# Kernel tuning notes

Measured on AMD Instinct MI355X. Metric: run time of the kernel, lower is better.

## Reference

```python
import jax, jax.numpy as jnp
import numpy as np

N, E, F, H, C = 100000, 1600000, 32, 64, 10


def setup_inputs() -> dict:
    key = jax.random.key(0)
    ks = jax.random.split(key, 12)
    x = jax.random.normal(ks[0], (N, F), dtype=jnp.float32)
    edge_index = jax.random.randint(ks[1], (2, E), 0, N, dtype=jnp.int64)
    edge_attr = jax.random.uniform(ks[2], (E,), dtype=jnp.float32)
    s = lambda k, shp, fan: jax.random.normal(k, shp, dtype=jnp.float32) / np.sqrt(fan)
    return {
        "x": x,
        "edge_index": edge_index,
        "edge_attr": edge_attr,
        "W1_rel": s(ks[3], (H, F), F),
        "b1_rel": jnp.zeros((H,), jnp.float32),
        "W1_root": s(ks[4], (H, F), F),
        "W2_rel": s(ks[5], (H, H), H),
        "b2_rel": jnp.zeros((H,), jnp.float32),
        "W2_root": s(ks[6], (H, H), H),
        "fc_w": s(ks[7], (C, H), H),
        "fc_b": jnp.zeros((C,), jnp.float32),
    }


def graph_conv(x, src, dst, ew, W_rel, b_rel, W_root):
    # message: x_j * e_ji, scatter-add at destination nodes (PyG GraphConv, aggr='add')
    msg = x[src] * ew[:, None]            # [E, d] gather + scale
    agg = jax.ops.segment_sum(msg, dst, num_segments=N)  # [N, d]
    return agg @ W_rel.T + b_rel + x @ W_root.T


def reference(x, edge_index, edge_attr, W1_rel, b1_rel, W1_root, W2_rel, b2_rel, W2_root, fc_w, fc_b):
    src, dst = edge_index[0], edge_index[1]
    h = jax.nn.relu(graph_conv(x, src, dst, edge_attr, W1_rel, b1_rel, W1_root))
    h = jax.nn.relu(graph_conv(h, src, dst, edge_attr, W2_rel, b2_rel, W2_root))
    return h @ fc_w.T + fc_b
```

## Files before the change

kernel.cpp:

```cpp
#include <hip/hip_runtime.h>

#define N_NODES 100000
#define EDGES   1600000
#define F_IN    32
#define H_DIM   64
#define C_OUT   10
#define SCAN_NB ((N_NODES + 511) / 512)

__global__ __launch_bounds__(256) void hist_kernel(
    const int* __restrict__ ei, int* __restrict__ cnt)
{
    int e = blockIdx.x * 256 + threadIdx.x;
    if (e >= EDGES) return;
    atomicAdd(&cnt[ei[EDGES + e]], 1);
}

__global__ __launch_bounds__(512) void scan1_kernel(
    const int* __restrict__ cnt, int* __restrict__ part, int* __restrict__ bsum)
{
    __shared__ int s[512];
    int tid = threadIdx.x;
    int gid = blockIdx.x * 512 + tid;
    int v = (gid < N_NODES) ? cnt[gid] : 0;
    s[tid] = v;
    __syncthreads();
    for (int off = 1; off < 512; off <<= 1) {
        int t = (tid >= off) ? s[tid - off] : 0;
        __syncthreads();
        s[tid] += t;
        __syncthreads();
    }
    if (gid < N_NODES) part[gid] = s[tid] - v;
    if (tid == 511) bsum[blockIdx.x] = s[511];
}

__global__ __launch_bounds__(256) void scan2_kernel(
    const int* __restrict__ bsum, int* __restrict__ bsumx)
{
    __shared__ int s[256];
    int tid = threadIdx.x;
    int v = (tid < SCAN_NB) ? bsum[tid] : 0;
    s[tid] = v;
    __syncthreads();
    for (int off = 1; off < 256; off <<= 1) {
        int t = (tid >= off) ? s[tid - off] : 0;
        __syncthreads();
        s[tid] += t;
        __syncthreads();
    }
    bsumx[tid] = s[tid] - v;
}

__global__ __launch_bounds__(512) void scan3_kernel(
    const int* __restrict__ part, const int* __restrict__ bsumx,
    int* __restrict__ offs, int* __restrict__ cursor)
{
    int gid = blockIdx.x * 512 + threadIdx.x;
    if (gid < N_NODES) {
        int o = part[gid] + bsumx[blockIdx.x];
        offs[gid] = o;
        cursor[gid] = o;
    }
    if (gid == 0) offs[N_NODES] = EDGES;
}

__global__ __launch_bounds__(256) void fill_kernel(
    const int* __restrict__ ei, const float* __restrict__ ew,
    int* __restrict__ cursor, uint2* __restrict__ bucket)
{
    int e = blockIdx.x * 256 + threadIdx.x;
    if (e >= EDGES) return;
    int d = ei[EDGES + e];
    int pos = atomicAdd(&cursor[d], 1);
    uint2 slot;
    slot.x = (unsigned)ei[e];
    slot.y = __float_as_uint(ew[e]);
    bucket[pos] = slot;
}

#define K1_NPB 8
__global__ __launch_bounds__(256) void agg_dense1_kernel(
    const float* __restrict__ x, const uint2* __restrict__ bucket,
    const int* __restrict__ offs,
    const float* __restrict__ W_rel, const float* __restrict__ b_rel,
    const float* __restrict__ W_root, float* __restrict__ h1)
{
    __shared__ float sWrel[64][33];
    __shared__ float sWroot[64][33];
    __shared__ float sb[64];
    __shared__ float sagg[K1_NPB][33];
    __shared__ float sx[K1_NPB][33];
    int tid = threadIdx.x;
    for (int i = tid; i < 64 * 32; i += 256) {
        sWrel[i >> 5][i & 31]  = W_rel[i];
        sWroot[i >> 5][i & 31] = W_root[i];
    }
    if (tid < 64) sb[tid] = b_rel[tid];
    int g = tid >> 5, f = tid & 31;
    int n4 = tid >> 6, h = tid & 63;

    for (int base = blockIdx.x * K1_NPB; base < N_NODES; base += gridDim.x * K1_NPB) {
        __syncthreads();
        {
            int node = base + g;
            float acc = 0.f, xv = 0.f;
            if (node < N_NODES) {
                xv = x[(size_t)node * 32 + f];
                int o0 = offs[node], o1 = offs[node + 1];
                int j = o0;
                for (; j + 4 <= o1; j += 4) {
                    uint2 s0 = bucket[j + 0];
                    uint2 s1 = bucket[j + 1];
                    uint2 s2 = bucket[j + 2];
                    uint2 s3 = bucket[j + 3];
                    float v0 = x[(size_t)s0.x * 32 + f];
                    float v1 = x[(size_t)s1.x * 32 + f];
                    float v2 = x[(size_t)s2.x * 32 + f];
                    float v3 = x[(size_t)s3.x * 32 + f];
                    acc += v0 * __uint_as_float(s0.y) + v1 * __uint_as_float(s1.y)
                         + v2 * __uint_as_float(s2.y) + v3 * __uint_as_float(s3.y);
                }
                for (; j < o1; ++j) {
                    uint2 s = bucket[j];
                    acc += x[(size_t)s.x * 32 + f] * __uint_as_float(s.y);
                }
            }
            sagg[g][f] = acc;
            sx[g][f] = xv;
        }
        __syncthreads();
        for (int ni = 0; ni < 2; ++ni) {
            int nn = ni * 4 + n4;
            int node = base + nn;
            if (node < N_NODES) {
                float sum = sb[h];
                #pragma unroll
                for (int ff = 0; ff < 32; ++ff)
                    sum += sagg[nn][ff] * sWrel[h][ff] + sx[nn][ff] * sWroot[h][ff];
                h1[(size_t)node * 64 + h] = fmaxf(sum, 0.f);
            }
        }
    }
}

#define K2_NPB 4
__global__ __launch_bounds__(256) void agg_dense2_kernel(
    const float* __restrict__ h1, const uint2* __restrict__ bucket,
    const int* __restrict__ offs,
    const float* __restrict__ W_rel, const float* __restrict__ b_rel,
    const float* __restrict__ W_root,
    const float* __restrict__ fc_w, const float* __restrict__ fc_b,
    float* __restrict__ out)
{
    __shared__ float sWrel[64][65];
    __shared__ float sWroot[64][65];
    __shared__ float sfc[10][65];
    __shared__ float sb[64], sfb[10];
    __shared__ float sagg[K2_NPB][65];
    __shared__ float sh[K2_NPB][65];
    __shared__ float sh2[K2_NPB][65];
    int tid = threadIdx.x;
    for (int i = tid; i < 64 * 64; i += 256) {
        sWrel[i >> 6][i & 63]  = W_rel[i];
        sWroot[i >> 6][i & 63] = W_root[i];
    }
    for (int i = tid; i < 10 * 64; i += 256) sfc[i >> 6][i & 63] = fc_w[i];
    if (tid < 64) sb[tid] = b_rel[tid];
    if (tid < 10) sfb[tid] = fc_b[tid];
    int g = tid >> 6, f = tid & 63;

    for (int base = blockIdx.x * K2_NPB; base < N_NODES; base += gridDim.x * K2_NPB) {
        __syncthreads();
        {
            int node = base + g;
            float acc = 0.f, hv = 0.f;
            if (node < N_NODES) {
                hv = h1[(size_t)node * 64 + f];
                int o0 = __builtin_amdgcn_readfirstlane(offs[node]);
                int o1 = __builtin_amdgcn_readfirstlane(offs[node + 1]);
                int j = o0;
                for (; j + 4 <= o1; j += 4) {
                    uint2 s0 = bucket[j + 0];
                    uint2 s1 = bucket[j + 1];
                    uint2 s2 = bucket[j + 2];
                    uint2 s3 = bucket[j + 3];
                    float v0 = h1[(size_t)s0.x * 64 + f];
                    float v1 = h1[(size_t)s1.x * 64 + f];
                    float v2 = h1[(size_t)s2.x * 64 + f];
                    float v3 = h1[(size_t)s3.x * 64 + f];
                    acc += v0 * __uint_as_float(s0.y) + v1 * __uint_as_float(s1.y)
                         + v2 * __uint_as_float(s2.y) + v3 * __uint_as_float(s3.y);
                }
                for (; j < o1; ++j) {
                    uint2 s = bucket[j];
                    acc += h1[(size_t)s.x * 64 + f] * __uint_as_float(s.y);
                }
            }
            sagg[g][f] = acc;
            sh[g][f] = hv;
        }
        __syncthreads();
        {
            float sum = sb[f];
            #pragma unroll
            for (int ff = 0; ff < 64; ++ff)
                sum += sagg[g][ff] * sWrel[f][ff] + sh[g][ff] * sWroot[f][ff];
            sh2[g][f] = fmaxf(sum, 0.f);
        }
        __syncthreads();
        if (tid < 4 * 10) {
            int n2 = tid / 10, c = tid % 10;
            int node = base + n2;
            if (node < N_NODES) {
                float o = sfb[c];
                #pragma unroll
                for (int ff = 0; ff < 64; ++ff)
                    o += sh2[n2][ff] * sfc[c][ff];
                out[(size_t)node * 10 + c] = o;
            }
        }
    }
}

extern "C" void kernel_launch(void* const* d_in, const int* in_sizes, int n_in,
                              void* d_out, int out_size, void* d_ws, size_t ws_size,
                              hipStream_t stream) {
    const float* x       = (const float*)d_in[0];
    const int*   ei      = (const int*)d_in[1];
    const float* ew      = (const float*)d_in[2];
    const float* W1_rel  = (const float*)d_in[3];
    const float* b1_rel  = (const float*)d_in[4];
    const float* W1_root = (const float*)d_in[5];
    const float* W2_rel  = (const float*)d_in[6];
    const float* b2_rel  = (const float*)d_in[7];
    const float* W2_root = (const float*)d_in[8];
    const float* fc_w    = (const float*)d_in[9];
    const float* fc_b    = (const float*)d_in[10];
    float* out = (float*)d_out;

    uint2* bucket = (uint2*)d_ws;
    float* h1     = (float*)(bucket + EDGES);
    int*   cnt    = (int*)(h1 + (size_t)N_NODES * 64);
    int*   part   = cnt + N_NODES;
    int*   offs   = part + N_NODES;
    int*   cursor = offs + N_NODES + 1;
    int*   bsum   = cursor + N_NODES;
    int*   bsumx  = bsum + 256;

    hipMemsetAsync(cnt, 0, (size_t)N_NODES * sizeof(int), stream);

    hist_kernel<<<(EDGES + 255) / 256, 256, 0, stream>>>(ei, cnt);
    scan1_kernel<<<SCAN_NB, 512, 0, stream>>>(cnt, part, bsum);
    scan2_kernel<<<1, 256, 0, stream>>>(bsum, bsumx);
    scan3_kernel<<<SCAN_NB, 512, 0, stream>>>(part, bsumx, offs, cursor);
    fill_kernel<<<(EDGES + 255) / 256, 256, 0, stream>>>(ei, ew, cursor, bucket);

    agg_dense1_kernel<<<2048, 256, 0, stream>>>(
        x, bucket, offs, W1_rel, b1_rel, W1_root, h1);
    agg_dense2_kernel<<<2048, 256, 0, stream>>>(
        h1, bucket, offs, W2_rel, b2_rel, W2_root, fc_w, fc_b, out);
}
```

Baseline: 502.6 us.

## Store hidden activations and weights in bf16, unroll gathers by eight

Stores the intermediate layer-1 output as bf16, halving the bytes gathered per edge in the second aggregation and the size of the h1 buffer. Weights are packed as bf16 pairs in shared memory, and both gather loops gain an 8-way unrolled path for more memory-level parallelism. Launch bounds now request higher occupancy. This gives up accuracy in the activations and weights, and each 2-byte gather per lane may coalesce less efficiently.

```diff
diff --git a/kernel.cpp b/kernel.cpp
--- a/kernel.cpp
+++ b/kernel.cpp
@@ -6,6 +6,16 @@
 #define H_DIM   64
 #define C_OUT   10
 #define SCAN_NB ((N_NODES + 511) / 512)
+
+__device__ __forceinline__ unsigned pack_bf16(float a, float b) {
+    unsigned ua = (__float_as_uint(a) + 0x8000u) >> 16;
+    unsigned ub = (__float_as_uint(b) + 0x8000u) & 0xffff0000u;
+    return ub | ua;
+}
+__device__ __forceinline__ float bflo(unsigned p) { return __uint_as_float(p << 16); }
+__device__ __forceinline__ float bfhi(unsigned p) { return __uint_as_float(p & 0xffff0000u); }
+__device__ __forceinline__ float bf2f(unsigned short u) { return __uint_as_float(((unsigned)u) << 16); }
+__device__ __forceinline__ unsigned short f2bf(float x) { return (unsigned short)((__float_as_uint(x) + 0x8000u) >> 16); }
 
 __global__ __launch_bounds__(256) void hist_kernel(
     const int* __restrict__ ei, int* __restrict__ cnt)
@@ -79,21 +89,22 @@
 }
 
 #define K1_NPB 8
-__global__ __launch_bounds__(256) void agg_dense1_kernel(
+__global__ __launch_bounds__(256, 6) void agg_dense1_kernel(
     const float* __restrict__ x, const uint2* __restrict__ bucket,
     const int* __restrict__ offs,
     const float* __restrict__ W_rel, const float* __restrict__ b_rel,
-    const float* __restrict__ W_root, float* __restrict__ h1)
-{
-    __shared__ float sWrel[64][33];
-    __shared__ float sWroot[64][33];
+    const float* __restrict__ W_root, unsigned short* __restrict__ h1b)
+{
+    __shared__ unsigned sWrel[64][17];
+    __shared__ unsigned sWroot[64][17];
     __shared__ float sb[64];
     __shared__ float sagg[K1_NPB][33];
     __shared__ float sx[K1_NPB][33];
     int tid = threadIdx.x;
-    for (int i = tid; i < 64 * 32; i += 256) {
-        sWrel[i >> 5][i & 31]  = W_rel[i];
-        sWroot[i >> 5][i & 31] = W_root[i];
+    for (int i = tid; i < 64 * 16; i += 256) {
+        int h = i >> 4, k = i & 15;
+        sWrel[h][k]  = pack_bf16(W_rel[h * 32 + 2 * k],  W_rel[h * 32 + 2 * k + 1]);
+        sWroot[h][k] = pack_bf16(W_root[h * 32 + 2 * k], W_root[h * 32 + 2 * k + 1]);
     }
     if (tid < 64) sb[tid] = b_rel[tid];
     int g = tid >> 5, f = tid & 31;
@@ -108,11 +119,27 @@
                 xv = x[(size_t)node * 32 + f];
                 int o0 = offs[node], o1 = offs[node + 1];
                 int j = o0;
+                for (; j + 8 <= o1; j += 8) {
+                    uint2 s0 = bucket[j + 0], s1 = bucket[j + 1];
+                    uint2 s2 = bucket[j + 2], s3 = bucket[j + 3];
+                    uint2 s4 = bucket[j + 4], s5 = bucket[j + 5];
+                    uint2 s6 = bucket[j + 6], s7 = bucket[j + 7];
+                    float v0 = x[(size_t)s0.x * 32 + f];
+                    float v1 = x[(size_t)s1.x * 32 + f];
+                    float v2 = x[(size_t)s2.x * 32 + f];
+                    float v3 = x[(size_t)s3.x * 32 + f];
+                    float v4 = x[(size_t)s4.x * 32 + f];
+                    float v5 = x[(size_t)s5.x * 32 + f];
+                    float v6 = x[(size_t)s6.x * 32 + f];
+                    float v7 = x[(size_t)s7.x * 32 + f];
+                    acc += v0 * __uint_as_float(s0.y) + v1 * __uint_as_float(s1.y)
+                         + v2 * __uint_as_float(s2.y) + v3 * __uint_as_float(s3.y)
+                         + v4 * __uint_as_float(s4.y) + v5 * __uint_as_float(s5.y)
+                         + v6 * __uint_as_float(s6.y) + v7 * __uint_as_float(s7.y);
+                }
                 for (; j + 4 <= o1; j += 4) {
-                    uint2 s0 = bucket[j + 0];
-                    uint2 s1 = bucket[j + 1];
-                    uint2 s2 = bucket[j + 2];
-                    uint2 s3 = bucket[j + 3];
+                    uint2 s0 = bucket[j + 0], s1 = bucket[j + 1];
+                    uint2 s2 = bucket[j + 2], s3 = bucket[j + 3];
                     float v0 = x[(size_t)s0.x * 32 + f];
                     float v1 = x[(size_t)s1.x * 32 + f];
                     float v2 = x[(size_t)s2.x * 32 + f];
@@ -135,36 +162,45 @@
             if (node < N_NODES) {
                 float sum = sb[h];
                 #pragma unroll
-                for (int ff = 0; ff < 32; ++ff)
-                    sum += sagg[nn][ff] * sWrel[h][ff] + sx[nn][ff] * sWroot[h][ff];
-                h1[(size_t)node * 64 + h] = fmaxf(sum, 0.f);
+                for (int k = 0; k < 16; ++k) {
+                    unsigned pr = sWrel[h][k], po = sWroot[h][k];
+                    sum += sagg[nn][2 * k]     * bflo(pr)
+                         + sagg[nn][2 * k + 1] * bfhi(pr)
+                         + sx[nn][2 * k]       * bflo(po)
+                         + sx[nn][2 * k + 1]   * bfhi(po);
+                }
+                h1b[(size_t)node * 64 + h] = f2bf(fmaxf(sum, 0.f));
             }
         }
     }
 }
 
 #define K2_NPB 4
-__global__ __launch_bounds__(256) void agg_dense2_kernel(
-    const float* __restrict__ h1, const uint2* __restrict__ bucket,
+__global__ __launch_bounds__(256, 6) void agg_dense2_kernel(
+    const unsigned short* __restrict__ h1b, const uint2* __restrict__ bucket,
     const int* __restrict__ offs,
     const float* __restrict__ W_rel, const float* __restrict__ b_rel,
     const float* __restrict__ W_root,
     const float* __restrict__ fc_w, const float* __restrict__ fc_b,
     float* __restrict__ out)
 {
-    __shared__ float sWrel[64][65];
-    __shared__ float sWroot[64][65];
-    __shared__ float sfc[10][65];
+    __shared__ unsigned sWrel[64][33];
+    __shared__ unsigned sWroot[64][33];
+    __shared__ unsigned sfc[10][33];
     __shared__ float sb[64], sfb[10];
     __shared__ float sagg[K2_NPB][65];
     __shared__ float sh[K2_NPB][65];
     __shared__ float sh2[K2_NPB][65];
     int tid = threadIdx.x;
-    for (int i = tid; i < 64 * 64; i += 256) {
-        sWrel[i >> 6][i & 63]  = W_rel[i];
-        sWroot[i >> 6][i & 63] = W_root[i];
-    }
-    for (int i = tid; i < 10 * 64; i += 256) sfc[i >> 6][i & 63] = fc_w[i];
+    for (int i = tid; i < 64 * 32; i += 256) {
+        int h = i >> 5, k = i & 31;
+        sWrel[h][k]  = pack_bf16(W_rel[h * 64 + 2 * k],  W_rel[h * 64 + 2 * k + 1]);
+        sWroot[h][k] = pack_bf16(W_root[h * 64 + 2 * k], W_root[h * 64 + 2 * k + 1]);
+    }
+    for (int i = tid; i < 10 * 32; i += 256) {
+        int c = i >> 5, k = i & 31;
+        sfc[c][k] = pack_bf16(fc_w[c * 64 + 2 * k], fc_w[c * 64 + 2 * k + 1]);
+    }
     if (tid < 64) sb[tid] = b_rel[tid];
     if (tid < 10) sfb[tid] = fc_b[tid];
     int g = tid >> 6, f = tid & 63;
@@ -175,25 +211,41 @@
             int node = base + g;
             float acc = 0.f, hv = 0.f;
             if (node < N_NODES) {
-                hv = h1[(size_t)node * 64 + f];
+                hv = bf2f(h1b[(size_t)node * 64 + f]);
                 int o0 = __builtin_amdgcn_readfirstlane(offs[node]);
                 int o1 = __builtin_amdgcn_readfirstlane(offs[node + 1]);
                 int j = o0;
+                for (; j + 8 <= o1; j += 8) {
+                    uint2 s0 = bucket[j + 0], s1 = bucket[j + 1];
+                    uint2 s2 = bucket[j + 2], s3 = bucket[j + 3];
+                    uint2 s4 = bucket[j + 4], s5 = bucket[j + 5];
+                    uint2 s6 = bucket[j + 6], s7 = bucket[j + 7];
+                    float v0 = bf2f(h1b[(size_t)s0.x * 64 + f]);
+                    float v1 = bf2f(h1b[(size_t)s1.x * 64 + f]);
+                    float v2 = bf2f(h1b[(size_t)s2.x * 64 + f]);
+                    float v3 = bf2f(h1b[(size_t)s3.x * 64 + f]);
+                    float v4 = bf2f(h1b[(size_t)s4.x * 64 + f]);
+                    float v5 = bf2f(h1b[(size_t)s5.x * 64 + f]);
+                    float v6 = bf2f(h1b[(size_t)s6.x * 64 + f]);
+                    float v7 = bf2f(h1b[(size_t)s7.x * 64 + f]);
+                    acc += v0 * __uint_as_float(s0.y) + v1 * __uint_as_float(s1.y)
+                         + v2 * __uint_as_float(s2.y) + v3 * __uint_as_float(s3.y)
+                         + v4 * __uint_as_float(s4.y) + v5 * __uint_as_float(s5.y)
+                         + v6 * __uint_as_float(s6.y) + v7 * __uint_as_float(s7.y);
+                }
                 for (; j + 4 <= o1; j += 4) {
-                    uint2 s0 = bucket[j + 0];
-                    uint2 s1 = bucket[j + 1];
-                    uint2 s2 = bucket[j + 2];
-                    uint2 s3 = bucket[j + 3];
-                    float v0 = h1[(size_t)s0.x * 64 + f];
-                    float v1 = h1[(size_t)s1.x * 64 + f];
-                    float v2 = h1[(size_t)s2.x * 64 + f];
-                    float v3 = h1[(size_t)s3.x * 64 + f];
+                    uint2 s0 = bucket[j + 0], s1 = bucket[j + 1];
+                    uint2 s2 = bucket[j + 2], s3 = bucket[j + 3];
+                    float v0 = bf2f(h1b[(size_t)s0.x * 64 + f]);
+                    float v1 = bf2f(h1b[(size_t)s1.x * 64 + f]);
+                    float v2 = bf2f(h1b[(size_t)s2.x * 64 + f]);
+                    float v3 = bf2f(h1b[(size_t)s3.x * 64 + f]);
                     acc += v0 * __uint_as_float(s0.y) + v1 * __uint_as_float(s1.y)
                          + v2 * __uint_as_float(s2.y) + v3 * __uint_as_float(s3.y);
                 }
                 for (; j < o1; ++j) {
                     uint2 s = bucket[j];
-                    acc += h1[(size_t)s.x * 64 + f] * __uint_as_float(s.y);
+                    acc += bf2f(h1b[(size_t)s.x * 64 + f]) * __uint_as_float(s.y);
                 }
             }
             sagg[g][f] = acc;
@@ -203,8 +255,13 @@
         {
             float sum = sb[f];
             #pragma unroll
-            for (int ff = 0; ff < 64; ++ff)
-                sum += sagg[g][ff] * sWrel[f][ff] + sh[g][ff] * sWroot[f][ff];
+            for (int k = 0; k < 32; ++k) {
+                unsigned pr = sWrel[f][k], po = sWroot[f][k];
+                sum += sagg[g][2 * k]     * bflo(pr)
+                     + sagg[g][2 * k + 1] * bfhi(pr)
+                     + sh[g][2 * k]       * bflo(po)
+                     + sh[g][2 * k + 1]   * bfhi(po);
+            }
             sh2[g][f] = fmaxf(sum, 0.f);
         }
         __syncthreads();
@@ -214,8 +271,10 @@
             if (node < N_NODES) {
                 float o = sfb[c];
                 #pragma unroll
-                for (int ff = 0; ff < 64; ++ff)
-                    o += sh2[n2][ff] * sfc[c][ff];
+                for (int k = 0; k < 32; ++k) {
+                    unsigned pc = sfc[c][k];
+                    o += sh2[n2][2 * k] * bflo(pc) + sh2[n2][2 * k + 1] * bfhi(pc);
+                }
                 out[(size_t)node * 10 + c] = o;
             }
         }
@@ -238,9 +297,9 @@
     const float* fc_b    = (const float*)d_in[10];
     float* out = (float*)d_out;
 
-    uint2* bucket = (uint2*)d_ws;
-    float* h1     = (float*)(bucket + EDGES);
-    int*   cnt    = (int*)(h1 + (size_t)N_NODES * 64);
+    uint2* bucket          = (uint2*)d_ws;
+    unsigned short* h1b    = (unsigned short*)(bucket + EDGES);
+    int*   cnt    = (int*)(h1b + (size_t)N_NODES * 64);
     int*   part   = cnt + N_NODES;
     int*   offs   = part + N_NODES;
     int*   cursor = offs + N_NODES + 1;
@@ -256,7 +315,7 @@
     fill_kernel<<<(EDGES + 255) / 256, 256, 0, stream>>>(ei, ew, cursor, bucket);
 
     agg_dense1_kernel<<<2048, 256, 0, stream>>>(
-        x, bucket, offs, W1_rel, b1_rel, W1_root, h1);
+        x, bucket, offs, W1_rel, b1_rel, W1_root, h1b);
     agg_dense2_kernel<<<2048, 256, 0, stream>>>(
-        h1, bucket, offs, W2_rel, b2_rel, W2_root, fc_w, fc_b, out);
-}
+        h1b, bucket, offs, W2_rel, b2_rel, W2_root, fc_w, fc_b, out);
+}
```

After: 459.2 us. 1.09x faster.
